# Kernel tuning notes

Hardware: AMD Instinct MI355X
Metric: run time of the kernel (lower is better)

Reference implementation:

```python
import jax, jax.numpy as jnp
import numpy as np

B, C, H, W = 16, 512, 32, 32
MID = max(8, C // 4)      # gate hidden
CA_MID = max(8, C // 4)   # channel-attn hidden
LOW_RADIUS = 0.35


def dct_mat(N):
    # Orthonormal DCT-II matrix: D[k,n] = s_k * sqrt(2/N) * cos(pi*(2n+1)*k/(2N))
    k = jnp.arange(N, dtype=jnp.float32)[:, None]
    n = jnp.arange(N, dtype=jnp.float32)[None, :]
    M = jnp.cos(jnp.pi * (2.0 * n + 1.0) * k / (2.0 * N)) * jnp.sqrt(2.0 / N)
    return M.at[0].multiply(1.0 / jnp.sqrt(2.0))


def build_low_mask(Hh, Ww, low_radius):
    yy = jnp.arange(Hh, dtype=jnp.float32)[:, None] / max(Hh - 1, 1)
    xx = jnp.arange(Ww, dtype=jnp.float32)[None, :] / max(Ww - 1, 1)
    rr = jnp.sqrt(yy ** 2 + xx ** 2)
    rr = rr / jnp.maximum(rr.max(), 1e-6)
    return (rr <= low_radius).astype(jnp.float32)[None, None]  # [1,1,H,W]


def conv1x1(x, w, b):
    # x: [B,Cin,H,W], w: [Cout,Cin], b: [Cout]
    return jnp.einsum('bchw,oc->bohw', x, w) + b[None, :, None, None]


def freq_transform(x, gw1, gb1, gw2, gb2, Dh, Dw, lm):
    # gate: avgpool -> 1x1 -> relu -> 1x1 -> sigmoid, output 2 scalars per sample
    pooled = jnp.mean(x, axis=(2, 3), keepdims=True)  # [B,C,1,1]
    g = jax.nn.sigmoid(conv1x1(jax.nn.relu(conv1x1(pooled, gw1, gb1)), gw2, gb2))
    g_low, g_high = g[:, 0:1], g[:, 1:2]  # [B,1,1,1]
    # 2D ortho DCT: Dh @ x @ Dw^T
    freq = jnp.einsum('ih,bchw->bciw', Dh, x)
    freq = jnp.einsum('jw,bchw->bchj', Dw, freq)
    # frequency gating fused
    gated = freq * (g_low * lm + g_high * (1.0 - lm))
    # inverse: Dh^T @ freq @ Dw
    out = jnp.einsum('hi,bchw->bciw', Dh, gated)
    out = jnp.einsum('wj,bchw->bchj', Dw, out)
    return out


def setup_inputs() -> dict:
    key = jax.random.key(0)
    ks = jax.random.split(key, 24)
    s = 1.0 / np.sqrt(C)
    d = {
        'rgb': jax.random.normal(ks[0], (B, C, H, W), jnp.float32),
        'dsm': jax.random.normal(ks[1], (B, C, H, W), jnp.float32),
        'rgb_w': jax.random.normal(ks[2], (C, C), jnp.float32) * s,
        'rgb_b': jax.random.normal(ks[3], (C,), jnp.float32) * 0.01,
        'dsm_w': jax.random.normal(ks[4], (C, C), jnp.float32) * s,
        'dsm_b': jax.random.normal(ks[5], (C,), jnp.float32) * 0.01,
        'gate_w1': jax.random.normal(ks[6], (MID, C), jnp.float32) * s,
        'gate_b1': jax.random.normal(ks[7], (MID,), jnp.float32) * 0.01,
        'gate_w2': jax.random.normal(ks[8], (2, MID), jnp.float32) * (1.0 / np.sqrt(MID)),
        'gate_b2': jax.random.normal(ks[9], (2,), jnp.float32) * 0.01,
        'q_w': jax.random.normal(ks[10], (C, C), jnp.float32) * s,
        'q_b': jax.random.normal(ks[11], (C,), jnp.float32) * 0.01,
        'k_w': jax.random.normal(ks[12], (C, C), jnp.float32) * s,
        'k_b': jax.random.normal(ks[13], (C,), jnp.float32) * 0.01,
        'v_w': jax.random.normal(ks[14], (C, C), jnp.float32) * s,
        'v_b': jax.random.normal(ks[15], (C,), jnp.float32) * 0.01,
        'sp_w': jax.random.normal(ks[16], (C, C, 3, 3), jnp.float32) * (s / 3.0),
        'sp_b': jax.random.normal(ks[17], (C,), jnp.float32) * 0.01,
        'ca_w1': jax.random.normal(ks[18], (CA_MID, C), jnp.float32) * s,
        'ca_b1': jax.random.normal(ks[19], (CA_MID,), jnp.float32) * 0.01,
        'ca_w2': jax.random.normal(ks[20], (C, CA_MID), jnp.float32) * (1.0 / np.sqrt(CA_MID)),
        'ca_b2': jax.random.normal(ks[21], (C,), jnp.float32) * 0.01,
    }
    return d


def reference(rgb, dsm, rgb_w, rgb_b, dsm_w, dsm_b, gate_w1, gate_b1, gate_w2, gate_b2,
              q_w, q_b, k_w, k_b, v_w, v_b, sp_w, sp_b, ca_w1, ca_b1, ca_w2, ca_b2):
    Dh, Dw = dct_mat(H), dct_mat(W)
    lm = build_low_mask(H, W, LOW_RADIUS)

    rgb_p = conv1x1(rgb, rgb_w, rgb_b)
    dsm_p = conv1x1(dsm, dsm_w, dsm_b)

    rgb_f = freq_transform(rgb_p, gate_w1, gate_b1, gate_w2, gate_b2, Dh, Dw, lm)
    dsm_f = freq_transform(dsm_p, gate_w1, gate_b1, gate_w2, gate_b2, Dh, Dw, lm)

    q = conv1x1(rgb_f, q_w, q_b).reshape(B, C, H * W)
    k = conv1x1(dsm_f, k_w, k_b).reshape(B, C, H * W)
    v = conv1x1(dsm_f, v_w, v_b).reshape(B, C, H * W)

    # attn over spatial tokens: [B,N,N]
    scores = jnp.einsum('bcn,bcm->bnm', q, k) / jnp.sqrt(jnp.float32(C))
    attn = jax.nn.softmax(scores, axis=-1)
    out = jnp.einsum('bnm,bcm->bcn', attn, v).reshape(B, C, H, W)

    spatial = jax.lax.conv_general_dilated(
        out, sp_w, window_strides=(1, 1), padding='SAME',
        dimension_numbers=('NCHW', 'OIHW', 'NCHW')) + sp_b[None, :, None, None]

    pooled = jnp.mean(spatial, axis=(2, 3), keepdims=True)
    weight = jax.nn.sigmoid(conv1x1(jax.nn.relu(conv1x1(pooled, ca_w1, ca_b1)), ca_w2, ca_b2))
    return rgb_p + spatial * weight
```

## Files before the change

kernel.cpp:

```cpp
#include <hip/hip_runtime.h>

typedef long long i64;
typedef unsigned int u32;
typedef unsigned short u16;

#define Bq 16
#define Cq 512
#define Hq 32
#define Wq 32
#define Nq 1024
#define MIDq 128
#define XPBq 591872

typedef __attribute__((ext_vector_type(8))) short bf16x8;
typedef __attribute__((ext_vector_type(4))) float f32x4;

static __device__ __forceinline__ u16 f2bf(float f) {
  u32 u = __float_as_uint(f);
  u = (u + 0x7FFFu + ((u >> 16) & 1u)) >> 16;
  return (u16)u;
}
static __device__ __forceinline__ float bf2f(u16 h) {
  return __uint_as_float(((u32)h) << 16);
}

__global__ __launch_bounds__(256) void k_prep(
    const float* __restrict__ rgb_w, const float* __restrict__ dsm_w,
    const float* __restrict__ q_w, const float* __restrict__ k_w,
    const float* __restrict__ v_w, const float* __restrict__ sp_w,
    u16* __restrict__ rw_h, u16* __restrict__ rw_l,
    u16* __restrict__ dw_h, u16* __restrict__ dw_l,
    u16* __restrict__ qw_h, u16* __restrict__ qw_l,
    u16* __restrict__ kw_h, u16* __restrict__ kw_l,
    u16* __restrict__ vw_h, u16* __restrict__ vw_l,
    u16* __restrict__ w9h, u16* __restrict__ w9l,
    float* __restrict__ Dm, float* __restrict__ lm) {
  int blk = blockIdx.x, tid = threadIdx.x;
  if (blk < 1280) {
    int wi = blk >> 8;
    const float* src = wi == 0 ? rgb_w : wi == 1 ? dsm_w : wi == 2 ? q_w : wi == 3 ? k_w : v_w;
    u16* hi = wi == 0 ? rw_h : wi == 1 ? dw_h : wi == 2 ? qw_h : wi == 3 ? kw_h : vw_h;
    u16* lo = wi == 0 ? rw_l : wi == 1 ? dw_l : wi == 2 ? qw_l : wi == 3 ? kw_l : vw_l;
    i64 idx = ((i64)(blk & 255) * 256 + tid) * 4;
    float4 f = *(const float4*)(src + idx);
    ushort4 h, l;
    h.x = f2bf(f.x); l.x = f2bf(f.x - bf2f(h.x));
    h.y = f2bf(f.y); l.y = f2bf(f.y - bf2f(h.y));
    h.z = f2bf(f.z); l.z = f2bf(f.z - bf2f(h.z));
    h.w = f2bf(f.w); l.w = f2bf(f.w - bf2f(h.w));
    *(ushort4*)(hi + idx) = h;
    *(ushort4*)(lo + idx) = l;
  } else if (blk < 1536) {
    int idx = (blk - 1280) * 256 + tid;
    int o = idx >> 7;
    int c4 = (idx & 127) << 2;
    float vals[4][9];
#pragma unroll
    for (int j = 0; j < 4; j++) {
      const float* wp = sp_w + ((i64)o * Cq + c4 + j) * 9;
#pragma unroll
      for (int t = 0; t < 9; t++) vals[j][t] = wp[t];
    }
#pragma unroll
    for (int t = 0; t < 9; t++) {
      ushort4 h, l;
      h.x = f2bf(vals[0][t]); l.x = f2bf(vals[0][t] - bf2f(h.x));
      h.y = f2bf(vals[1][t]); l.y = f2bf(vals[1][t] - bf2f(h.y));
      h.z = f2bf(vals[2][t]); l.z = f2bf(vals[2][t] - bf2f(h.z));
      h.w = f2bf(vals[3][t]); l.w = f2bf(vals[3][t] - bf2f(h.w));
      i64 od = (i64)t * (Cq * Cq) + (i64)o * Cq + c4;
      *(ushort4*)(w9h + od) = h;
      *(ushort4*)(w9l + od) = l;
    }
  } else {
#pragma unroll
    for (int q4 = 0; q4 < 4; q4++) {
      int t = tid * 4 + q4;
      int i = t >> 5, j = t & 31;
      float v = cosf(3.14159265358979323846f * (2.0f * j + 1.0f) * (float)i / 64.0f) * 0.25f;
      if (i == 0) v *= 0.7071067811865476f;
      Dm[t] = v;
      float yy = i * (1.0f / 31.0f), xx = j * (1.0f / 31.0f);
      float rr = sqrtf(yy * yy + xx * xx) * 0.7071067811865476f;
      lm[t] = (rr <= 0.35f) ? 1.0f : 0.0f;
    }
  }
}

__global__ __launch_bounds__(64) void k_zero_border(u16* __restrict__ xp) {
  int i = blockIdx.x;
  int b = blockIdx.y;
  int arr = blockIdx.z;
  int pr;
  if (i < 34) pr = i;
  else if (i < 68) pr = 33 * 34 + (i - 34);
  else { int j = i - 68; pr = (1 + (j >> 1)) * 34 + (j & 1) * 33; }
  u16* p = xp + (i64)arr * ((i64)Bq * XPBq) + (i64)b * XPBq + (i64)pr * Cq;
  *(uint4*)(p + threadIdx.x * 8) = (uint4){0u, 0u, 0u, 0u};
}

__global__ __launch_bounds__(256) void k_padsplit_t(
    const float* __restrict__ src, u16* __restrict__ hi, u16* __restrict__ lo) {
  __shared__ float ld[64][65];
  int b = blockIdx.z;
  int c0 = blockIdx.y << 6;
  int n0 = blockIdx.x << 6;
  int tid = threadIdx.x;
  const float* s = src + (i64)b * (Cq * Nq);
  u16* ph = hi + (i64)b * XPBq;
  u16* pl = lo + (i64)b * XPBq;
#pragma unroll
  for (int p = 0; p < 4; p++) {
    int row = (tid >> 4) + p * 16;
    int col4 = (tid & 15) << 2;
    *(float4*)&ld[row][col4] = *(const float4*)(s + (i64)(c0 + row) * Nq + n0 + col4);
  }
  __syncthreads();
#pragma unroll
  for (int p = 0; p < 4; p++) {
    int nr = (tid >> 4) + p * 16;
    int c4 = (tid & 15) << 2;
    float f0 = ld[c4 + 0][nr], f1 = ld[c4 + 1][nr];
    float f2 = ld[c4 + 2][nr], f3 = ld[c4 + 3][nr];
    ushort4 h, l;
    h.x = f2bf(f0); l.x = f2bf(f0 - bf2f(h.x));
    h.y = f2bf(f1); l.y = f2bf(f1 - bf2f(h.y));
    h.z = f2bf(f2); l.z = f2bf(f2 - bf2f(h.z));
    h.w = f2bf(f3); l.w = f2bf(f3 - bf2f(h.w));
    int n = n0 + nr;
    int pr = ((n >> 5) + 1) * 34 + (n & 31) + 1;
    i64 o = (i64)pr * Cq + c0 + c4;
    *(ushort4*)(ph + o) = h;
    *(ushort4*)(pl + o) = l;
  }
}

__global__ __launch_bounds__(256) void k_gemm(
    const u16* __restrict__ Ahi, const u16* __restrict__ Alo,
    const float* __restrict__ Af32, int a_mode, i64 sAb,
    const u16* __restrict__ Bhi, const u16* __restrict__ Blo,
    const float* __restrict__ Bf32, int b_mode, i64 sBb,
    const float* __restrict__ bias, int bias_mode, float scale,
    int M, int N, int K,
    float* __restrict__ Cf, u16* __restrict__ Chi, u16* __restrict__ Clo,
    i64 sCb, int out_mode) {
  __shared__ __align__(16) u16 As_h[128][40];
  __shared__ __align__(16) u16 As_l[128][40];
  __shared__ __align__(16) u16 Bs_h[128][40];
  __shared__ __align__(16) u16 Bs_l[128][40];
  int tid = threadIdx.x;
  int gx = gridDim.x, gxy = gx * gridDim.y;
  int nwg = gxy * gridDim.z;
  int orig = blockIdx.x + gx * blockIdx.y + gxy * blockIdx.z;
  int wg = (nwg & 7) ? orig : ((orig & 7) * (nwg >> 3) + (orig >> 3));
  int b = wg / gxy;
  int rem = wg - b * gxy;
  int m0 = (rem / gx) << 7;
  int n0 = (rem - (rem / gx) * gx) << 7;
  const u16* pAhi = Ahi + (i64)b * (a_mode ? 0 : sAb);
  const u16* pAlo = Alo + (i64)b * (a_mode ? 0 : sAb);
  const float* pAf = a_mode ? (Af32 + (i64)b * sAb) : nullptr;
  const u16* pBhi = Bhi + (i64)b * (b_mode ? 0 : sBb);
  const u16* pBlo = Blo + (i64)b * (b_mode ? 0 : sBb);
  const float* pBf = b_mode ? (Bf32 + (i64)b * sBb) : nullptr;
  int lane = tid & 63;
  int wid = tid >> 6;
  int wm = (wid & 1) << 6;
  int wn = (wid >> 1) << 6;
  int l15 = lane & 15;
  int g8 = (lane >> 4) << 3;
  f32x4 acc[4][4];
#pragma unroll
  for (int mi = 0; mi < 4; mi++)
#pragma unroll
    for (int nj = 0; nj < 4; nj++)
      acc[mi][nj] = (f32x4){0.f, 0.f, 0.f, 0.f};

  for (int k0 = 0; k0 < K; k0 += 32) {
    if (a_mode == 0) {
#pragma unroll
      for (int i = 0; i < 4; i++) {
        int r = ((i & 1) << 6) + (tid >> 2);
        int seg = tid & 3;
        const u16* src = (i < 2) ? pAhi : pAlo;
        uint4 val = *(const uint4*)(src + (i64)(m0 + r) * K + k0 + seg * 8);
        if (i < 2) *(uint4*)&As_h[r][seg * 8] = val;
        else       *(uint4*)&As_l[r][seg * 8] = val;
      }
    } else {
      int cs = tid >> 6, ns = tid & 63;
      const float* src = pAf + (i64)(k0 + cs * 8) * M + m0 + ns * 2;
      float2 f[8];
#pragma unroll
      for (int j = 0; j < 8; j++) f[j] = *(const float2*)(src + (i64)j * M);
#pragma unroll
      for (int i = 0; i < 2; i++) {
        union { u16 u[8]; uint4 v; } hh, ll;
#pragma unroll
        for (int j = 0; j < 8; j++) {
          float x = i ? f[j].y : f[j].x;
          u16 h = f2bf(x);
          hh.u[j] = h;
          ll.u[j] = (u16)(__float_as_uint(x - bf2f(h)) >> 16);
        }
        *(uint4*)&As_h[2 * ns + i][8 * cs] = hh.v;
        *(uint4*)&As_l[2 * ns + i][8 * cs] = ll.v;
      }
    }
    if (b_mode == 0) {
#pragma unroll
      for (int i = 0; i < 4; i++) {
        int r = ((i & 1) << 6) + (tid >> 2);
        int seg = tid & 3;
        const u16* src = (i < 2) ? pBhi : pBlo;
        uint4 val = *(const uint4*)(src + (i64)(n0 + r) * K + k0 + seg * 8);
        if (i < 2) *(uint4*)&Bs_h[r][seg * 8] = val;
        else       *(uint4*)&Bs_l[r][seg * 8] = val;
      }
    } else {
      int cs = tid >> 6, ns = tid & 63;
      const float* src = pBf + (i64)(k0 + cs * 8) * N + n0 + ns * 2;
      float2 f[8];
#pragma unroll
      for (int j = 0; j < 8; j++) f[j] = *(const float2*)(src + (i64)j * N);
#pragma unroll
      for (int i = 0; i < 2; i++) {
        union { u16 u[8]; uint4 v; } hh, ll;
#pragma unroll
        for (int j = 0; j < 8; j++) {
          float x = i ? f[j].y : f[j].x;
          u16 h = f2bf(x);
          hh.u[j] = h;
          ll.u[j] = (u16)(__float_as_uint(x - bf2f(h)) >> 16);
        }
        *(uint4*)&Bs_h[2 * ns + i][8 * cs] = hh.v;
        *(uint4*)&Bs_l[2 * ns + i][8 * cs] = ll.v;
      }
    }
    __syncthreads();
    bf16x8 ah[4], al[4], bh[4], bl[4];
#pragma unroll
    for (int mi = 0; mi < 4; mi++) {
      int row = wm + mi * 16 + l15;
      ah[mi] = *(const bf16x8*)&As_h[row][g8];
      al[mi] = *(const bf16x8*)&As_l[row][g8];
    }
#pragma unroll
    for (int nj = 0; nj < 4; nj++) {
      int row = wn + nj * 16 + l15;
      bh[nj] = *(const bf16x8*)&Bs_h[row][g8];
      bl[nj] = *(const bf16x8*)&Bs_l[row][g8];
    }
#pragma unroll
    for (int mi = 0; mi < 4; mi++)
#pragma unroll
      for (int nj = 0; nj < 4; nj++) {
        acc[mi][nj] = __builtin_amdgcn_mfma_f32_16x16x32_bf16(ah[mi], bh[nj], acc[mi][nj], 0, 0, 0);
        acc[mi][nj] = __builtin_amdgcn_mfma_f32_16x16x32_bf16(ah[mi], bl[nj], acc[mi][nj], 0, 0, 0);
        acc[mi][nj] = __builtin_amdgcn_mfma_f32_16x16x32_bf16(al[mi], bh[nj], acc[mi][nj], 0, 0, 0);
      }
    __syncthreads();
  }

#pragma unroll
  for (int mi = 0; mi < 4; mi++)
#pragma unroll
    for (int nj = 0; nj < 4; nj++) {
      int col_g = n0 + wn + nj * 16 + l15;
#pragma unroll
      for (int r = 0; r < 4; r++) {
        int row_g = m0 + wm + mi * 16 + ((lane >> 4) << 2) + r;
        float val = acc[mi][nj][r] * scale;
        if (bias_mode == 1) val += bias[row_g];
        else if (bias_mode == 2) val += bias[col_g];
        i64 o = (i64)b * sCb + (i64)row_g * N + col_g;
        if (out_mode == 0) {
          Cf[o] = val;
        } else {
          u16 h = f2bf(val);
          Chi[o] = h;
          Clo[o] = f2bf(val - bf2f(h));
        }
      }
    }
}

__global__ __launch_bounds__(256) void k_conv3_mfma(
    const u16* __restrict__ Wh, const u16* __restrict__ Wl,
    const u16* __restrict__ Xh, const u16* __restrict__ Xl,
    const float* __restrict__ bias, float* __restrict__ out) {
  __shared__ __align__(16) u16 As_h[128][40];
  __shared__ __align__(16) u16 As_l[128][40];
  __shared__ __align__(16) u16 Bs_h[128][40];
  __shared__ __align__(16) u16 Bs_l[128][40];
  int tid = threadIdx.x;
  int gx = gridDim.x, gxy = gx * gridDim.y;
  int nwg = gxy * gridDim.z;
  int orig = blockIdx.x + gx * blockIdx.y + gxy * blockIdx.z;
  int wg = (nwg & 7) ? orig : ((orig & 7) * (nwg >> 3) + (orig >> 3));
  int b = wg / gxy;
  int rem = wg - b * gxy;
  int m0 = (rem / gx) << 7;
  int n0 = (rem - (rem / gx) * gx) << 7;
  const u16* pXh = Xh + (i64)b * XPBq;
  const u16* pXl = Xl + (i64)b * XPBq;
  int lane = tid & 63;
  int wid = tid >> 6;
  int wm = (wid & 1) << 6;
  int wn = (wid >> 1) << 6;
  int l15 = lane & 15;
  int g8 = (lane >> 4) << 3;
  int rr = tid >> 2, seg = tid & 3;
  int n_a = n0 + rr, n_b = n0 + 64 + rr;
  int prb0 = (n_a >> 5) * 34 + (n_a & 31);
  int prb1 = (n_b >> 5) * 34 + (n_b & 31);
  f32x4 acc[4][4];
#pragma unroll
  for (int mi = 0; mi < 4; mi++)
#pragma unroll
    for (int nj = 0; nj < 4; nj++)
      acc[mi][nj] = (f32x4){0.f, 0.f, 0.f, 0.f};

  for (int tap = 0; tap < 9; tap++) {
    int doff = (tap / 3) * 34 + (tap % 3);
    const u16* wth = Wh + (i64)tap * (Cq * Cq);
    const u16* wtl = Wl + (i64)tap * (Cq * Cq);
    i64 bb0 = (i64)(prb0 + doff) * Cq + seg * 8;
    i64 bb1 = (i64)(prb1 + doff) * Cq + seg * 8;
    for (int c0 = 0; c0 < Cq; c0 += 32) {
      *(uint4*)&As_h[rr][seg * 8]      = *(const uint4*)(wth + (i64)(m0 + rr) * Cq + c0 + seg * 8);
      *(uint4*)&As_h[64 + rr][seg * 8] = *(const uint4*)(wth + (i64)(m0 + 64 + rr) * Cq + c0 + seg * 8);
      *(uint4*)&As_l[rr][seg * 8]      = *(const uint4*)(wtl + (i64)(m0 + rr) * Cq + c0 + seg * 8);
      *(uint4*)&As_l[64 + rr][seg * 8] = *(const uint4*)(wtl + (i64)(m0 + 64 + rr) * Cq + c0 + seg * 8);
      *(uint4*)&Bs_h[rr][seg * 8]      = *(const uint4*)(pXh + bb0 + c0);
      *(uint4*)&Bs_h[64 + rr][seg * 8] = *(const uint4*)(pXh + bb1 + c0);
      *(uint4*)&Bs_l[rr][seg * 8]      = *(const uint4*)(pXl + bb0 + c0);
      *(uint4*)&Bs_l[64 + rr][seg * 8] = *(const uint4*)(pXl + bb1 + c0);
      __syncthreads();
      bf16x8 ah[4], al[4], bh[4], bl[4];
#pragma unroll
      for (int mi = 0; mi < 4; mi++) {
        int row = wm + mi * 16 + l15;
        ah[mi] = *(const bf16x8*)&As_h[row][g8];
        al[mi] = *(const bf16x8*)&As_l[row][g8];
      }
#pragma unroll
      for (int nj = 0; nj < 4; nj++) {
        int row = wn + nj * 16 + l15;
        bh[nj] = *(const bf16x8*)&Bs_h[row][g8];
        bl[nj] = *(const bf16x8*)&Bs_l[row][g8];
      }
#pragma unroll
      for (int mi = 0; mi < 4; mi++)
#pragma unroll
        for (int nj = 0; nj < 4; nj++) {
          acc[mi][nj] = __builtin_amdgcn_mfma_f32_16x16x32_bf16(ah[mi], bh[nj], acc[mi][nj], 0, 0, 0);
          acc[mi][nj] = __builtin_amdgcn_mfma_f32_16x16x32_bf16(ah[mi], bl[nj], acc[mi][nj], 0, 0, 0);
          acc[mi][nj] = __builtin_amdgcn_mfma_f32_16x16x32_bf16(al[mi], bh[nj], acc[mi][nj], 0, 0, 0);
        }
      __syncthreads();
    }
  }

#pragma unroll
  for (int mi = 0; mi < 4; mi++)
#pragma unroll
    for (int nj = 0; nj < 4; nj++) {
      int col_g = n0 + wn + nj * 16 + l15;
#pragma unroll
      for (int r = 0; r < 4; r++) {
        int row_g = m0 + wm + mi * 16 + ((lane >> 4) << 2) + r;
        float val = acc[mi][nj][r] + bias[row_g];
        out[(i64)b * (Cq * Nq) + (i64)row_g * Nq + col_g] = val;
      }
    }
}

__global__ __launch_bounds__(256) void k_pool(const float* __restrict__ x, float* __restrict__ o) {
  int gw = (int)((blockIdx.x * 256 + threadIdx.x) >> 6);
  int ln = threadIdx.x & 63;
  const float* p = x + (i64)gw * Nq;
  float s = 0.f;
#pragma unroll
  for (int it = 0; it < 4; it++) {
    float4 v = *(const float4*)(p + ln * 4 + it * 256);
    s += v.x + v.y + v.z + v.w;
  }
#pragma unroll
  for (int off = 32; off > 0; off >>= 1) s += __shfl_xor(s, off, 64);
  if (ln == 0) o[gw] = s * (1.0f / 1024.0f);
}

__global__ __launch_bounds__(128) void k_gate(
    const float* __restrict__ pooled, const float* __restrict__ w1,
    const float* __restrict__ b1, const float* __restrict__ w2,
    const float* __restrict__ b2, float* __restrict__ g) {
  __shared__ float pl[Cq];
  __shared__ float h[MIDq];
  int bb = blockIdx.x, tid = threadIdx.x;
  for (int c = tid; c < Cq; c += 128) pl[c] = pooled[bb * Cq + c];
  __syncthreads();
  float s = b1[tid];
  const float* wr = w1 + (i64)tid * Cq;
  for (int c = 0; c < Cq; c++) s = fmaf(wr[c], pl[c], s);
  h[tid] = fmaxf(s, 0.f);
  __syncthreads();
  if (tid < 2) {
    float t = b2[tid];
    const float* w2r = w2 + tid * MIDq;
    for (int m = 0; m < MIDq; m++) t = fmaf(w2r[m], h[m], t);
    g[bb * 2 + tid] = 1.0f / (1.0f + expf(-t));
  }
}

__global__ __launch_bounds__(256) void k_freq(
    const float* __restrict__ xr, const float* __restrict__ xd,
    float* __restrict__ yr, float* __restrict__ yd,
    const float* __restrict__ g_r, const float* __restrict__ g_d,
    const float* __restrict__ Dm, const float* __restrict__ lm) {
  __shared__ float Ds[32][36], Dt[32][36], Xs[32][36], T1[32][36];
  int bid = blockIdx.x;
  const float* x; float* y; const float* g;
  if (bid < Bq * Cq) {
    x = xr + (i64)bid * Nq; y = yr + (i64)bid * Nq; g = g_r + (bid >> 9) * 2;
  } else {
    int id = bid - Bq * Cq;
    x = xd + (i64)id * Nq; y = yd + (i64)id * Nq; g = g_d + (id >> 9) * 2;
  }
  int tid = threadIdx.x;
  int r_ = tid >> 3, j4 = (tid & 7) << 2;
  {
    float4 dv = *(const float4*)(Dm + tid * 4);
    *(float4*)&Ds[r_][j4] = dv;
    Dt[j4 + 0][r_] = dv.x; Dt[j4 + 1][r_] = dv.y;
    Dt[j4 + 2][r_] = dv.z; Dt[j4 + 3][r_] = dv.w;
    *(float4*)&Xs[r_][j4] = *(const float4*)(x + tid * 4);
  }
  float gl = g[0], gh = g[1];
  __syncthreads();
  float a0 = 0, a1 = 0, a2 = 0, a3 = 0;
#pragma unroll
  for (int h = 0; h < 32; h++) {
    float a = Ds[r_][h];
    float4 bv = *(const float4*)&Xs[h][j4];
    a0 = fmaf(a, bv.x, a0); a1 = fmaf(a, bv.y, a1);
    a2 = fmaf(a, bv.z, a2); a3 = fmaf(a, bv.w, a3);
  }
  *(float4*)&T1[r_][j4] = make_float4(a0, a1, a2, a3);
  __syncthreads();
  a0 = a1 = a2 = a3 = 0;
#pragma unroll
  for (int w = 0; w < 32; w++) {
    float a = T1[r_][w];
    float4 bv = *(const float4*)&Dt[w][j4];
    a0 = fmaf(a, bv.x, a0); a1 = fmaf(a, bv.y, a1);
    a2 = fmaf(a, bv.z, a2); a3 = fmaf(a, bv.w, a3);
  }
  {
    float4 mv = *(const float4*)(lm + r_ * 32 + j4);
    a0 *= fmaf(gl, mv.x, gh * (1.f - mv.x));
    a1 *= fmaf(gl, mv.y, gh * (1.f - mv.y));
    a2 *= fmaf(gl, mv.z, gh * (1.f - mv.z));
    a3 *= fmaf(gl, mv.w, gh * (1.f - mv.w));
  }
  __syncthreads();
  *(float4*)&Xs[r_][j4] = make_float4(a0, a1, a2, a3);
  __syncthreads();
  a0 = a1 = a2 = a3 = 0;
#pragma unroll
  for (int ii = 0; ii < 32; ii++) {
    float a = Dt[r_][ii];
    float4 bv = *(const float4*)&Xs[ii][j4];
    a0 = fmaf(a, bv.x, a0); a1 = fmaf(a, bv.y, a1);
    a2 = fmaf(a, bv.z, a2); a3 = fmaf(a, bv.w, a3);
  }
  __syncthreads();
  *(float4*)&T1[r_][j4] = make_float4(a0, a1, a2, a3);
  __syncthreads();
  a0 = a1 = a2 = a3 = 0;
#pragma unroll
  for (int jj = 0; jj < 32; jj++) {
    float a = T1[r_][jj];
    float4 bv = *(const float4*)&Ds[jj][j4];
    a0 = fmaf(a, bv.x, a0); a1 = fmaf(a, bv.y, a1);
    a2 = fmaf(a, bv.z, a2); a3 = fmaf(a, bv.w, a3);
  }
  *(float4*)(y + tid * 4) = make_float4(a0, a1, a2, a3);
}

__global__ __launch_bounds__(256) void k_softmax_split(
    const float* __restrict__ sc, u16* __restrict__ ahi, u16* __restrict__ alo) {
  __shared__ float redm[4], reds[4];
  i64 row = blockIdx.x;
  const float* p = sc + row * (i64)Nq;
  int tid = threadIdx.x;
  float4 v = ((const float4*)p)[tid];
  float mx = fmaxf(fmaxf(v.x, v.y), fmaxf(v.z, v.w));
#pragma unroll
  for (int o = 32; o > 0; o >>= 1) mx = fmaxf(mx, __shfl_xor(mx, o, 64));
  if ((tid & 63) == 0) redm[tid >> 6] = mx;
  __syncthreads();
  mx = fmaxf(fmaxf(redm[0], redm[1]), fmaxf(redm[2], redm[3]));
  v.x = expf(v.x - mx); v.y = expf(v.y - mx);
  v.z = expf(v.z - mx); v.w = expf(v.w - mx);
  float s = v.x + v.y + v.z + v.w;
#pragma unroll
  for (int o = 32; o > 0; o >>= 1) s += __shfl_xor(s, o, 64);
  if ((tid & 63) == 0) reds[tid >> 6] = s;
  __syncthreads();
  s = reds[0] + reds[1] + reds[2] + reds[3];
  float inv = 1.0f / s;
  v.x *= inv; v.y *= inv; v.z *= inv; v.w *= inv;
  ushort4 h, l;
  h.x = f2bf(v.x); l.x = f2bf(v.x - bf2f(h.x));
  h.y = f2bf(v.y); l.y = f2bf(v.y - bf2f(h.y));
  h.z = f2bf(v.z); l.z = f2bf(v.z - bf2f(h.z));
  h.w = f2bf(v.w); l.w = f2bf(v.w - bf2f(h.w));
  *(ushort4*)(ahi + row * Nq + tid * 4) = h;
  *(ushort4*)(alo + row * Nq + tid * 4) = l;
}

__global__ __launch_bounds__(512) void k_ca(
    const float* __restrict__ pooled, const float* __restrict__ w1,
    const float* __restrict__ b1, const float* __restrict__ w2,
    const float* __restrict__ b2, float* __restrict__ wt) {
  __shared__ float pl[Cq];
  __shared__ float h[MIDq];
  int b = blockIdx.x, tid = threadIdx.x;
  pl[tid] = pooled[b * Cq + tid];
  __syncthreads();
  if (tid < MIDq) {
    float s = b1[tid];
    const float* wr = w1 + (i64)tid * Cq;
    for (int c = 0; c < Cq; c++) s = fmaf(wr[c], pl[c], s);
    h[tid] = fmaxf(s, 0.f);
  }
  __syncthreads();
  float s = b2[tid];
  const float* wr = w2 + (i64)tid * MIDq;
  for (int m = 0; m < MIDq; m++) s = fmaf(wr[m], h[m], s);
  wt[b * Cq + tid] = 1.0f / (1.0f + expf(-s));
}

__global__ __launch_bounds__(256) void k_final(
    const float* __restrict__ rgbp, const float* __restrict__ sp,
    const float* __restrict__ wt, float* __restrict__ out) {
  i64 idx = (i64)blockIdx.x * 256 + threadIdx.x;
  float4 a = ((const float4*)rgbp)[idx];
  float4 s = ((const float4*)sp)[idx];
  float w = wt[idx >> 8];
  float4 r;
  r.x = fmaf(s.x, w, a.x); r.y = fmaf(s.y, w, a.y);
  r.z = fmaf(s.z, w, a.z); r.w = fmaf(s.w, w, a.w);
  ((float4*)out)[idx] = r;
}

extern "C" void kernel_launch(void* const* d_in, const int* in_sizes, int n_in,
                              void* d_out, int out_size, void* d_ws, size_t ws_size,
                              hipStream_t stream) {
  (void)in_sizes; (void)n_in; (void)out_size; (void)ws_size;
  const float* rgb    = (const float*)d_in[0];
  const float* dsm    = (const float*)d_in[1];
  const float* rgb_w  = (const float*)d_in[2];
  const float* rgb_b  = (const float*)d_in[3];
  const float* dsm_w  = (const float*)d_in[4];
  const float* dsm_b  = (const float*)d_in[5];
  const float* gate_w1 = (const float*)d_in[6];
  const float* gate_b1 = (const float*)d_in[7];
  const float* gate_w2 = (const float*)d_in[8];
  const float* gate_b2 = (const float*)d_in[9];
  const float* q_w = (const float*)d_in[10];
  const float* q_b = (const float*)d_in[11];
  const float* k_w = (const float*)d_in[12];
  const float* k_b = (const float*)d_in[13];
  const float* v_w = (const float*)d_in[14];
  const float* v_b = (const float*)d_in[15];
  const float* sp_w = (const float*)d_in[16];
  const float* sp_b = (const float*)d_in[17];
  const float* ca_w1 = (const float*)d_in[18];
  const float* ca_b1 = (const float*)d_in[19];
  const float* ca_w2 = (const float*)d_in[20];
  const float* ca_b2 = (const float*)d_in[21];

  const i64 S  = (i64)Bq * Cq * Nq;
  const i64 SU = S;
  const i64 WE = (i64)Cq * Cq;
  const i64 XPT = (i64)Bq * XPBq;

  float* wsf = (float*)d_ws;
  float* rgbp   = wsf;
  float* dsmp   = wsf + S;
  float* rgbf   = wsf + 2 * S;
  float* dsmf   = wsf + 3 * S;
  float* scores  = dsmp;
  float* attout  = dsmf;
  float* spatial = dsmp;
  float* smallr = wsf + 4 * S;
  float* Dm     = smallr;
  float* lm     = smallr + 1024;
  float* pooled = smallr + 2048;
  float* g_all  = smallr + 18432;
  float* wt     = smallr + 18496;
  u16* ub = (u16*)(wsf + 4 * S + 32768);
  u16* U0 = ub;          u16* U1 = ub + SU;
  u16* U2 = ub + 2 * SU; u16* U3 = ub + 3 * SU;
  u16* U4 = ub + 4 * SU; u16* U5 = ub + 5 * SU;
  (void)U1; (void)U3; (void)U5;
  u16* XPh = ub;
  u16* XPl = ub + XPT;
  u16* wb = ub + 6 * SU;
  u16* rgbw_h = wb;           u16* rgbw_l = wb + WE;
  u16* dsmw_h = wb + 2 * WE;  u16* dsmw_l = wb + 3 * WE;
  u16* qw_h   = wb + 4 * WE;  u16* qw_l   = wb + 5 * WE;
  u16* kw_h   = wb + 6 * WE;  u16* kw_l   = wb + 7 * WE;
  u16* vw_h   = wb + 8 * WE;  u16* vw_l   = wb + 9 * WE;
  u16* w9h    = wb + 10 * WE; u16* w9l    = wb + 19 * WE;

  const i64 sT = (i64)Nq * Cq;
  const i64 sS = (i64)Nq * Nq;
  const float rsqc = 0.044194173824159216f;

  k_prep<<<1537, 256, 0, stream>>>(rgb_w, dsm_w, q_w, k_w, v_w, sp_w,
                                   rgbw_h, rgbw_l, dsmw_h, dsmw_l, qw_h, qw_l,
                                   kw_h, kw_l, vw_h, vw_l, w9h, w9l, Dm, lm);

  dim3 gW(Nq / 128, Cq / 128, Bq);
  dim3 gQ(Cq / 128, Nq / 128, Bq);
  dim3 gS(Nq / 128, Nq / 128, Bq);

  k_gemm<<<gW, 256, 0, stream>>>(rgbw_h, rgbw_l, nullptr, 0, 0,
                                 nullptr, nullptr, rgb, 1, sT,
                                 rgb_b, 1, 1.0f, Cq, Nq, Cq,
                                 rgbp, nullptr, nullptr, sT, 0);
  k_gemm<<<gW, 256, 0, stream>>>(dsmw_h, dsmw_l, nullptr, 0, 0,
                                 nullptr, nullptr, dsm, 1, sT,
                                 dsm_b, 1, 1.0f, Cq, Nq, Cq,
                                 dsmp, nullptr, nullptr, sT, 0);

  k_pool<<<(2 * Bq * Cq) / 4, 256, 0, stream>>>(rgbp, pooled);
  k_gate<<<32, 128, 0, stream>>>(pooled, gate_w1, gate_b1, gate_w2, gate_b2, g_all);

  k_freq<<<2 * Bq * Cq, 256, 0, stream>>>(rgbp, dsmp, rgbf, dsmf, g_all, g_all + 32, Dm, lm);

  k_gemm<<<gQ, 256, 0, stream>>>(nullptr, nullptr, rgbf, 1, sT,
                                 qw_h, qw_l, nullptr, 0, 0,
                                 q_b, 2, 1.0f, Nq, Cq, Cq,
                                 nullptr, U4, U5, sT, 1);
  k_gemm<<<gQ, 256, 0, stream>>>(nullptr, nullptr, dsmf, 1, sT,
                                 kw_h, kw_l, nullptr, 0, 0,
                                 k_b, 2, 1.0f, Nq, Cq, Cq,
                                 nullptr, U0, U1, sT, 1);
  k_gemm<<<gS, 256, 0, stream>>>(U4, U5, nullptr, 0, sT,
                                 U0, U1, nullptr, 0, sT,
                                 nullptr, 0, rsqc, Nq, Nq, Cq,
                                 scores, nullptr, nullptr, sS, 0);
  k_gemm<<<gW, 256, 0, stream>>>(vw_h, vw_l, nullptr, 0, 0,
                                 nullptr, nullptr, dsmf, 1, sT,
                                 v_b, 1, 1.0f, Cq, Nq, Cq,
                                 nullptr, U4, U5, sT, 1);
  k_softmax_split<<<Bq * Nq, 256, 0, stream>>>(scores, U0, U2);
  k_gemm<<<gW, 256, 0, stream>>>(U4, U5, nullptr, 0, sT,
                                 U0, U2, nullptr, 0, sS,
                                 nullptr, 0, 1.0f, Cq, Nq, Nq,
                                 attout, nullptr, nullptr, sT, 0);

  k_zero_border<<<dim3(132, Bq, 2), 64, 0, stream>>>(XPh);
  k_padsplit_t<<<dim3(Nq / 64, Cq / 64, Bq), 256, 0, stream>>>(attout, XPh, XPl);
  k_conv3_mfma<<<dim3(Nq / 128, Cq / 128, Bq), 256, 0, stream>>>(
      w9h, w9l, XPh, XPl, sp_b, spatial);

  k_pool<<<(Bq * Cq) / 4, 256, 0, stream>>>(spatial, pooled);
  k_ca<<<Bq, 512, 0, stream>>>(pooled, ca_w1, ca_b1, ca_w2, ca_b2, wt);

  k_final<<<(int)(S / 4 / 256), 256, 0, stream>>>(rgbp, spatial, wt, (float*)d_out);
}
```

Baseline: 783.9 us.

## Fuse pad/split transpose into attention GEMM epilogue; deepen conv K-tile to 64

The attn@V GEMM now writes its output straight into the padded, transposed hi/lo bf16 buffers through a new epilogue mode. This removes the separate k_padsplit_t pass and the fp32 attout round trip. The 3x3 conv kernel also loads 64 channels per shared-memory stage instead of 32, which halves the number of barriers per tap but uses more LDS. The fused epilogue writes ushort4 values with a channel-major stride, so those stores may coalesce poorly, and the workspace buffers are reassigned to hold the padded data in dsmp.

```diff
diff --git a/kernel.cpp b/kernel.cpp
--- a/kernel.cpp
+++ b/kernel.cpp
@@ -97,42 +97,6 @@
   else { int j = i - 68; pr = (1 + (j >> 1)) * 34 + (j & 1) * 33; }
   u16* p = xp + (i64)arr * ((i64)Bq * XPBq) + (i64)b * XPBq + (i64)pr * Cq;
   *(uint4*)(p + threadIdx.x * 8) = (uint4){0u, 0u, 0u, 0u};
-}
-
-__global__ __launch_bounds__(256) void k_padsplit_t(
-    const float* __restrict__ src, u16* __restrict__ hi, u16* __restrict__ lo) {
-  __shared__ float ld[64][65];
-  int b = blockIdx.z;
-  int c0 = blockIdx.y << 6;
-  int n0 = blockIdx.x << 6;
-  int tid = threadIdx.x;
-  const float* s = src + (i64)b * (Cq * Nq);
-  u16* ph = hi + (i64)b * XPBq;
-  u16* pl = lo + (i64)b * XPBq;
-#pragma unroll
-  for (int p = 0; p < 4; p++) {
-    int row = (tid >> 4) + p * 16;
-    int col4 = (tid & 15) << 2;
-    *(float4*)&ld[row][col4] = *(const float4*)(s + (i64)(c0 + row) * Nq + n0 + col4);
-  }
-  __syncthreads();
-#pragma unroll
-  for (int p = 0; p < 4; p++) {
-    int nr = (tid >> 4) + p * 16;
-    int c4 = (tid & 15) << 2;
-    float f0 = ld[c4 + 0][nr], f1 = ld[c4 + 1][nr];
-    float f2 = ld[c4 + 2][nr], f3 = ld[c4 + 3][nr];
-    ushort4 h, l;
-    h.x = f2bf(f0); l.x = f2bf(f0 - bf2f(h.x));
-    h.y = f2bf(f1); l.y = f2bf(f1 - bf2f(h.y));
-    h.z = f2bf(f2); l.z = f2bf(f2 - bf2f(h.z));
-    h.w = f2bf(f3); l.w = f2bf(f3 - bf2f(h.w));
-    int n = n0 + nr;
-    int pr = ((n >> 5) + 1) * 34 + (n & 31) + 1;
-    i64 o = (i64)pr * Cq + c0 + c4;
-    *(ushort4*)(ph + o) = h;
-    *(ushort4*)(pl + o) = l;
-  }
 }
 
 __global__ __launch_bounds__(256) void k_gemm(
@@ -267,20 +231,37 @@
 #pragma unroll
     for (int nj = 0; nj < 4; nj++) {
       int col_g = n0 + wn + nj * 16 + l15;
+      int row_b = m0 + wm + mi * 16 + ((lane >> 4) << 2);
+      float v4[4];
 #pragma unroll
       for (int r = 0; r < 4; r++) {
-        int row_g = m0 + wm + mi * 16 + ((lane >> 4) << 2) + r;
         float val = acc[mi][nj][r] * scale;
-        if (bias_mode == 1) val += bias[row_g];
+        if (bias_mode == 1) val += bias[row_b + r];
         else if (bias_mode == 2) val += bias[col_g];
-        i64 o = (i64)b * sCb + (i64)row_g * N + col_g;
-        if (out_mode == 0) {
-          Cf[o] = val;
-        } else {
-          u16 h = f2bf(val);
+        v4[r] = val;
+      }
+      if (out_mode == 0) {
+#pragma unroll
+        for (int r = 0; r < 4; r++)
+          Cf[(i64)b * sCb + (i64)(row_b + r) * N + col_g] = v4[r];
+      } else if (out_mode == 1) {
+#pragma unroll
+        for (int r = 0; r < 4; r++) {
+          i64 o = (i64)b * sCb + (i64)(row_b + r) * N + col_g;
+          u16 h = f2bf(v4[r]);
           Chi[o] = h;
-          Clo[o] = f2bf(val - bf2f(h));
+          Clo[o] = f2bf(v4[r] - bf2f(h));
         }
+      } else {
+        int pr = ((col_g >> 5) + 1) * 34 + (col_g & 31) + 1;
+        i64 o = (i64)b * sCb + (i64)pr * Cq + row_b;
+        ushort4 hh, ll;
+        hh.x = f2bf(v4[0]); ll.x = f2bf(v4[0] - bf2f(hh.x));
+        hh.y = f2bf(v4[1]); ll.y = f2bf(v4[1] - bf2f(hh.y));
+        hh.z = f2bf(v4[2]); ll.z = f2bf(v4[2] - bf2f(hh.z));
+        hh.w = f2bf(v4[3]); ll.w = f2bf(v4[3] - bf2f(hh.w));
+        *(ushort4*)(Chi + o) = hh;
+        *(ushort4*)(Clo + o) = ll;
       }
     }
 }
@@ -289,10 +270,10 @@
     const u16* __restrict__ Wh, const u16* __restrict__ Wl,
     const u16* __restrict__ Xh, const u16* __restrict__ Xl,
     const float* __restrict__ bias, float* __restrict__ out) {
-  __shared__ __align__(16) u16 As_h[128][40];
-  __shared__ __align__(16) u16 As_l[128][40];
-  __shared__ __align__(16) u16 Bs_h[128][40];
-  __shared__ __align__(16) u16 Bs_l[128][40];
+  __shared__ __align__(16) u16 As_h[128][72];
+  __shared__ __align__(16) u16 As_l[128][72];
+  __shared__ __align__(16) u16 Bs_h[128][72];
+  __shared__ __align__(16) u16 Bs_l[128][72];
   int tid = threadIdx.x;
   int gx = gridDim.x, gxy = gx * gridDim.y;
   int nwg = gxy * gridDim.z;
@@ -325,39 +306,48 @@
     int doff = (tap / 3) * 34 + (tap % 3);
     const u16* wth = Wh + (i64)tap * (Cq * Cq);
     const u16* wtl = Wl + (i64)tap * (Cq * Cq);
-    i64 bb0 = (i64)(prb0 + doff) * Cq + seg * 8;
-    i64 bb1 = (i64)(prb1 + doff) * Cq + seg * 8;
-    for (int c0 = 0; c0 < Cq; c0 += 32) {
-      *(uint4*)&As_h[rr][seg * 8]      = *(const uint4*)(wth + (i64)(m0 + rr) * Cq + c0 + seg * 8);
-      *(uint4*)&As_h[64 + rr][seg * 8] = *(const uint4*)(wth + (i64)(m0 + 64 + rr) * Cq + c0 + seg * 8);
-      *(uint4*)&As_l[rr][seg * 8]      = *(const uint4*)(wtl + (i64)(m0 + rr) * Cq + c0 + seg * 8);
-      *(uint4*)&As_l[64 + rr][seg * 8] = *(const uint4*)(wtl + (i64)(m0 + 64 + rr) * Cq + c0 + seg * 8);
-      *(uint4*)&Bs_h[rr][seg * 8]      = *(const uint4*)(pXh + bb0 + c0);
-      *(uint4*)&Bs_h[64 + rr][seg * 8] = *(const uint4*)(pXh + bb1 + c0);
-      *(uint4*)&Bs_l[rr][seg * 8]      = *(const uint4*)(pXl + bb0 + c0);
-      *(uint4*)&Bs_l[64 + rr][seg * 8] = *(const uint4*)(pXl + bb1 + c0);
+    i64 bb0 = (i64)(prb0 + doff) * Cq;
+    i64 bb1 = (i64)(prb1 + doff) * Cq;
+    for (int c0 = 0; c0 < Cq; c0 += 64) {
+#pragma unroll
+      for (int half = 0; half < 2; half++) {
+        int col = seg * 8 + half * 32;
+        i64 gc = c0 + col;
+        *(uint4*)&As_h[rr][col]      = *(const uint4*)(wth + (i64)(m0 + rr) * Cq + gc);
+        *(uint4*)&As_h[64 + rr][col] = *(const uint4*)(wth + (i64)(m0 + 64 + rr) * Cq + gc);
+        *(uint4*)&As_l[rr][col]      = *(const uint4*)(wtl + (i64)(m0 + rr) * Cq + gc);
+        *(uint4*)&As_l[64 + rr][col] = *(const uint4*)(wtl + (i64)(m0 + 64 + rr) * Cq + gc);
+        *(uint4*)&Bs_h[rr][col]      = *(const uint4*)(pXh + bb0 + gc);
+        *(uint4*)&Bs_h[64 + rr][col] = *(const uint4*)(pXh + bb1 + gc);
+        *(uint4*)&Bs_l[rr][col]      = *(const uint4*)(pXl + bb0 + gc);
+        *(uint4*)&Bs_l[64 + rr][col] = *(const uint4*)(pXl + bb1 + gc);
+      }
       __syncthreads();
-      bf16x8 ah[4], al[4], bh[4], bl[4];
-#pragma unroll
-      for (int mi = 0; mi < 4; mi++) {
-        int row = wm + mi * 16 + l15;
-        ah[mi] = *(const bf16x8*)&As_h[row][g8];
-        al[mi] = *(const bf16x8*)&As_l[row][g8];
-      }
-#pragma unroll
-      for (int nj = 0; nj < 4; nj++) {
-        int row = wn + nj * 16 + l15;
-        bh[nj] = *(const bf16x8*)&Bs_h[row][g8];
-        bl[nj] = *(const bf16x8*)&Bs_l[row][g8];
-      }
-#pragma unroll
-      for (int mi = 0; mi < 4; mi++)
+#pragma unroll
+      for (int ks = 0; ks < 2; ks++) {
+        int gk = ks * 32 + g8;
+        bf16x8 ah[4], al[4], bh[4], bl[4];
+#pragma unroll
+        for (int mi = 0; mi < 4; mi++) {
+          int row = wm + mi * 16 + l15;
+          ah[mi] = *(const bf16x8*)&As_h[row][gk];
+          al[mi] = *(const bf16x8*)&As_l[row][gk];
+        }
 #pragma unroll
         for (int nj = 0; nj < 4; nj++) {
-          acc[mi][nj] = __builtin_amdgcn_mfma_f32_16x16x32_bf16(ah[mi], bh[nj], acc[mi][nj], 0, 0, 0);
-          acc[mi][nj] = __builtin_amdgcn_mfma_f32_16x16x32_bf16(ah[mi], bl[nj], acc[mi][nj], 0, 0, 0);
-          acc[mi][nj] = __builtin_amdgcn_mfma_f32_16x16x32_bf16(al[mi], bh[nj], acc[mi][nj], 0, 0, 0);
+          int row = wn + nj * 16 + l15;
+          bh[nj] = *(const bf16x8*)&Bs_h[row][gk];
+          bl[nj] = *(const bf16x8*)&Bs_l[row][gk];
         }
+#pragma unroll
+        for (int mi = 0; mi < 4; mi++)
+#pragma unroll
+          for (int nj = 0; nj < 4; nj++) {
+            acc[mi][nj] = __builtin_amdgcn_mfma_f32_16x16x32_bf16(ah[mi], bh[nj], acc[mi][nj], 0, 0, 0);
+            acc[mi][nj] = __builtin_amdgcn_mfma_f32_16x16x32_bf16(ah[mi], bl[nj], acc[mi][nj], 0, 0, 0);
+            acc[mi][nj] = __builtin_amdgcn_mfma_f32_16x16x32_bf16(al[mi], bh[nj], acc[mi][nj], 0, 0, 0);
+          }
+      }
       __syncthreads();
     }
   }
@@ -593,8 +583,9 @@
   float* rgbf   = wsf + 2 * S;
   float* dsmf   = wsf + 3 * S;
   float* scores  = dsmp;
-  float* attout  = dsmf;
-  float* spatial = dsmp;
+  float* spatial = dsmf;
+  u16* XPh = (u16*)dsmp;
+  u16* XPl = XPh + XPT;
   float* smallr = wsf + 4 * S;
   float* Dm     = smallr;
   float* lm     = smallr + 1024;
@@ -603,11 +594,8 @@
   float* wt     = smallr + 18496;
   u16* ub = (u16*)(wsf + 4 * S + 32768);
   u16* U0 = ub;          u16* U1 = ub + SU;
-  u16* U2 = ub + 2 * SU; u16* U3 = ub + 3 * SU;
+  u16* U2 = ub + 2 * SU;
   u16* U4 = ub + 4 * SU; u16* U5 = ub + 5 * SU;
-  (void)U1; (void)U3; (void)U5;
-  u16* XPh = ub;
-  u16* XPl = ub + XPT;
   u16* wb = ub + 6 * SU;
   u16* rgbw_h = wb;           u16* rgbw_l = wb + WE;
   u16* dsmw_h = wb + 2 * WE;  u16* dsmw_l = wb + 3 * WE;
@@ -659,13 +647,12 @@
                                  v_b, 1, 1.0f, Cq, Nq, Cq,
                                  nullptr, U4, U5, sT, 1);
   k_softmax_split<<<Bq * Nq, 256, 0, stream>>>(scores, U0, U2);
+  k_zero_border<<<dim3(132, Bq, 2), 64, 0, stream>>>(XPh);
   k_gemm<<<gW, 256, 0, stream>>>(U4, U5, nullptr, 0, sT,
                                  U0, U2, nullptr, 0, sS,
                                  nullptr, 0, 1.0f, Cq, Nq, Nq,
-                                 attout, nullptr, nullptr, sT, 0);
-
-  k_zero_border<<<dim3(132, Bq, 2), 64, 0, stream>>>(XPh);
-  k_padsplit_t<<<dim3(Nq / 64, Cq / 64, Bq), 256, 0, stream>>>(attout, XPh, XPl);
+                                 nullptr, XPh, XPl, XPBq, 2);
+
   k_conv3_mfma<<<dim3(Nq / 128, Cq / 128, Bq), 256, 0, stream>>>(
       w9h, w9l, XPh, XPl, sp_b, spatial);
 
```

Result: faster. 758.9 us (-3.2%).
